# Kernel tuning notes

Measured on AMD Instinct MI355X. Metric: run time of the kernel, lower is better.

Reference implementation:

```python
import jax, jax.numpy as jnp
import numpy as np

N, E, B = 524288, 4194304, 16384
F_IN, FP, TV, GOUT = 14, 1024, 256, 32
EPS = 1e-5
SLOPE = 0.2  # PyG GATConv default negative_slope


def setup_inputs() -> dict:
    key = jax.random.key(0)
    ks = iter(jax.random.split(key, 64))
    def nrm(shape, scale=1.0):
        return jax.random.normal(next(ks), shape, dtype=jnp.float32) * scale
    def uni(shape, lo, hi):
        return jax.random.uniform(next(ks), shape, dtype=jnp.float32, minval=lo, maxval=hi)
    def bn(d):  # [gamma, beta, running_mean, running_var]
        return jnp.stack([uni((d,), 0.5, 1.5), nrm((d,), 0.1), nrm((d,), 0.1), uni((d,), 0.5, 1.5)])
    return {
        'x': nrm((N, F_IN)),
        'edge_index': jax.random.randint(next(ks), (2, E), 0, N, dtype=jnp.int32),
        'batch': jnp.sort(jax.random.randint(next(ks), (N,), 0, B, dtype=jnp.int32)),
        'fingerprint': nrm((B, FP)),
        'transformer_features': nrm((B, TV)),
        'W1': nrm((F_IN, F_IN), 0.3), 'a_src1': nrm((F_IN,), 0.3), 'a_dst1': nrm((F_IN,), 0.3), 'b1': nrm((F_IN,), 0.1),
        'W2': nrm((F_IN, GOUT), 0.3), 'a_src2': nrm((GOUT,), 0.3), 'a_dst2': nrm((GOUT,), 0.3), 'b2': nrm((GOUT,), 0.1),
        'fc1_w': nrm((FP, 400), 0.04), 'fc1_b': nrm((400,), 0.1), 'bn1': bn(400),
        'fc2_w': nrm((400, 200), 0.07), 'fc2_b': nrm((200,), 0.1), 'bn2': bn(200),
        'fc3_w': nrm((TV, 400), 0.08), 'fc3_b': nrm((400,), 0.1), 'bn3': bn(400),
        'fc4_w': nrm((400, 200), 0.07), 'fc4_b': nrm((200,), 0.1), 'bn4': bn(200),
        'fcc1_w': nrm((GOUT + 400, 100), 0.07), 'fcc1_b': nrm((100,), 0.1), 'bnc': bn(100),
        'fcc2_w': nrm((100, 1), 0.1), 'fcc2_b': nrm((1,), 0.1),
    }


def _bn(h, p):  # eval-mode BatchNorm1d with packed params [4, d]
    return (h - p[2]) * jax.lax.rsqrt(p[3] + EPS) * p[0] + p[1]


def _gat(x, W, a_s, a_d, b, src, dst, n):
    # PyG GATConv, heads=1: messages flow src -> dst, softmax over incoming edges per dst
    h = x @ W                                   # [n, C]
    e = jax.nn.leaky_relu((h @ a_s)[src] + (h @ a_d)[dst], SLOPE)  # [E_tot]
    m = jax.lax.stop_gradient(jax.ops.segment_max(e, dst, num_segments=n))
    w = jnp.exp(e - m[dst])
    denom = jax.ops.segment_sum(w, dst, num_segments=n)
    alpha = w / denom[dst]
    out = jax.ops.segment_sum(alpha[:, None] * h[src], dst, num_segments=n)
    return out + b


def reference(x, edge_index, batch, fingerprint, transformer_features,
              W1, a_src1, a_dst1, b1, W2, a_src2, a_dst2, b2,
              fc1_w, fc1_b, bn1, fc2_w, fc2_b, bn2,
              fc3_w, fc3_b, bn3, fc4_w, fc4_b, bn4,
              fcc1_w, fcc1_b, bnc, fcc2_w, fcc2_b):
    n = x.shape[0]
    loop = jnp.arange(n, dtype=edge_index.dtype)  # add_self_loops
    src = jnp.concatenate([edge_index[0], loop])
    dst = jnp.concatenate([edge_index[1], loop])
    g = jax.nn.relu(_gat(x, W1, a_src1, a_dst1, b1, src, dst, n))
    g = jax.nn.relu(_gat(g, W2, a_src2, a_dst2, b2, src, dst, n))
    pool = jax.ops.segment_sum(g, batch, num_segments=B)  # global_add_pool -> [B, GOUT]
    fp = jax.nn.relu(_bn(fingerprint @ fc1_w + fc1_b, bn1))
    fp = jax.nn.relu(_bn(fp @ fc2_w + fc2_b, bn2))
    tv = jax.nn.relu(_bn(transformer_features @ fc3_w + fc3_b, bn3))
    tv = jax.nn.relu(_bn(tv @ fc4_w + fc4_b, bn4))
    comb = jnp.concatenate([pool, fp, tv], axis=1)  # [B, 32+200+200]
    comb = jax.nn.relu(_bn(comb @ fcc1_w + fcc1_b, bnc))
    return comb @ fcc2_w + fcc2_b  # [B, 1]
```

## Files before the change

kernel.cpp:

```cpp
#include <hip/hip_runtime.h>

typedef unsigned short u16;
typedef unsigned int u32;
typedef __attribute__((ext_vector_type(8))) short bf16x8;
typedef __attribute__((ext_vector_type(4))) float f32x4;

#define N_NODES 524288
#define N_EDGES 4194304
#define N_GRAPH 16384
#define P_BLOCKS 1024
#define BKTS 512
#define DPB 1024
#define CAP 8960

__device__ __forceinline__ float bf2f(u16 u){ u32 x=((u32)u)<<16; float f; __builtin_memcpy(&f,&x,4); return f; }
__device__ __forceinline__ float lo2f(u32 u){ u32 x=u<<16; float f; __builtin_memcpy(&f,&x,4); return f; }
__device__ __forceinline__ float hi2f(u32 u){ u32 x=u&0xffff0000u; float f; __builtin_memcpy(&f,&x,4); return f; }
__device__ __forceinline__ u16 f2bf(float f){ u32 x; __builtin_memcpy(&x,&f,4); return (u16)((x + 0x7fffu + ((x>>16)&1u))>>16); }
__device__ __forceinline__ float lrelu(float e){ return e>0.f? e : 0.2f*e; }
__device__ __forceinline__ float gload(const void* p, int i, int is32){
    return is32 ? ((const float*)p)[i] : bf2f(((const u16*)p)[i]);
}
__device__ __forceinline__ u32 fmax_key(float f){ u32 u; __builtin_memcpy(&u,&f,4); return (u>>31)? ~u : (u|0x80000000u); }
__device__ __forceinline__ float key_fmax(u32 k){ u32 u = (k>>31)? (k^0x80000000u) : ~k; float f; __builtin_memcpy(&f,&u,4); return f; }

__device__ __forceinline__ void edge_acc(uint4 q0, uint4 q1, float adv, float M,
        float* acc, float& den){
    float as_; __builtin_memcpy(&as_, &q1.w, 4);
    float w = __expf(lrelu(as_ + adv) - M); den += w;
    u32 u[7] = {q0.x,q0.y,q0.z,q0.w,q1.x,q1.y,q1.z};
    #pragma unroll
    for (int f=0;f<14;f++){ u32 uu=u[f>>1]; acc[f] += w*((f&1)? hi2f(uu):lo2f(uu)); }
}

__device__ __forceinline__ void walk8(const int* __restrict__ ssrc, const u16* __restrict__ hsrc,
        int beg, int end, float adv, float M, float* acc, float& den){
    for (int j = beg; j < end; j += 8){
        int s8[8];
        #pragma unroll
        for (int k=0;k<8;k++){
            int e = j + k;
            s8[k] = __builtin_nontemporal_load(ssrc + ((e < end) ? e : (end-1)));
        }
        uint4 r0[8], r1[8];
        #pragma unroll
        for (int k=0;k<8;k++){
            const uint4* hp = (const uint4*)(hsrc + (size_t)s8[k]*16);
            r0[k] = hp[0]; r1[k] = hp[1];
        }
        int m = end - j;
        #pragma unroll
        for (int k=0;k<8;k++) if (k < m) edge_acc(r0[k], r1[k], adv, M, acc, den);
    }
}

__global__ __launch_bounds__(256) void k_detect(const u32* __restrict__ x, int* __restrict__ flag,
        const void* __restrict__ W2, const void* __restrict__ asw, const void* __restrict__ adw,
        float* __restrict__ prep){
    __shared__ int cnt, s32;
    int t = threadIdx.x;
    if (t==0) cnt = 0;
    __syncthreads();
    int c = 0;
    for (int i = t; i < 1024; i += 256){
        u32 e = (x[i] >> 7) & 0xFF;
        if (e >= 110 && e <= 140) c++;
    }
    atomicAdd(&cnt, c);
    __syncthreads();
    if (t==0){ int f = (cnt < 512) ? 1 : 0; *flag = f; s32 = f; }
    __syncthreads();
    int is32 = s32;
    if (t < 28){
        int j = t % 14, which = t / 14;
        const void* av = which ? adw : asw;
        float s = 0.f;
        #pragma unroll
        for (int k=0;k<32;k++) s += gload(W2, j*32+k, is32) * gload(av, k, is32);
        prep[which*14 + j] = s;
    }
}

__global__ __launch_bounds__(256) void k_cast(const void* __restrict__ in, u16* __restrict__ out,
        int n8, const int* __restrict__ flag){
    int is32 = *flag;
    int idx = blockIdx.x*256 + threadIdx.x;
    if (idx >= n8) return;
    if (is32){
        const float4* ip = (const float4*)in + idx*2;
        float4 a0 = ip[0], a1 = ip[1];
        u32 w0 = (u32)f2bf(a0.x) | ((u32)f2bf(a0.y)<<16);
        u32 w1 = (u32)f2bf(a0.z) | ((u32)f2bf(a0.w)<<16);
        u32 w2 = (u32)f2bf(a1.x) | ((u32)f2bf(a1.y)<<16);
        u32 w3 = (u32)f2bf(a1.z) | ((u32)f2bf(a1.w)<<16);
        ((uint4*)out)[idx] = make_uint4(w0,w1,w2,w3);
    } else {
        ((uint4*)out)[idx] = ((const uint4*)in)[idx];
    }
}

__global__ __launch_bounds__(256) void k_p1(const int* __restrict__ dst, u32* __restrict__ tbl_bm){
    __shared__ u32 lh[BKTS];
    int t = threadIdx.x, blk = blockIdx.x;
    lh[t] = 0; lh[t+256] = 0;
    __syncthreads();
    int base = blk*4096;
    #pragma unroll
    for (int k=0;k<16;k++){
        int d = __builtin_nontemporal_load(dst + base + k*256 + t) & (N_NODES-1);
        atomicAdd(&lh[d>>10], 1);
    }
    __syncthreads();
    tbl_bm[blk*BKTS + t]       = lh[t];
    tbl_bm[blk*BKTS + t + 256] = lh[t+256];
}

__global__ __launch_bounds__(256) void k_ttbl(const u32* __restrict__ bm, u32* __restrict__ km){
    __shared__ u32 tile[32][33];
    int bx = blockIdx.x, by = blockIdx.y;
    int tx = threadIdx.x & 31, ty = threadIdx.x >> 5;
    #pragma unroll
    for (int r=0;r<32;r+=8)
        tile[ty+r][tx] = bm[(bx*32 + ty + r)*BKTS + by*32 + tx];
    __syncthreads();
    #pragma unroll
    for (int r=0;r<32;r+=8)
        km[(by*32 + ty + r)*P_BLOCKS + bx*32 + tx] = tile[tx][ty+r];
}

__global__ __launch_bounds__(256) void k_scan1(int* __restrict__ data, int* __restrict__ bsums){
    __shared__ int sh[256];
    int b = blockIdx.x, t = threadIdx.x;
    int base = b*1024 + t*4;
    int4 v = *(const int4*)(data + base);
    int s = v.x+v.y+v.z+v.w;
    sh[t] = s; __syncthreads();
    for (int off=1; off<256; off<<=1){
        int xv = (t>=off)? sh[t-off] : 0; __syncthreads();
        sh[t] += xv; __syncthreads();
    }
    int excl = sh[t] - s;
    if (t==255) bsums[b] = sh[255];
    int4 o; o.x = excl; o.y = excl+v.x; o.z = o.y+v.y; o.w = o.z+v.z;
    *(int4*)(data + base) = o;
}

__global__ __launch_bounds__(256) void k_scan2(int* __restrict__ bsums){
    __shared__ int sh[256];
    int t = threadIdx.x;
    int v0 = bsums[2*t], v1 = bsums[2*t+1];
    int s = v0+v1; sh[t] = s; __syncthreads();
    for (int off=1; off<256; off<<=1){
        int xv = (t>=off)? sh[t-off] : 0; __syncthreads();
        sh[t] += xv; __syncthreads();
    }
    int excl = sh[t] - s;
    bsums[2*t] = excl; bsums[2*t+1] = excl + v0;
}

__global__ __launch_bounds__(256) void k_scan3(int* __restrict__ scan, const int* __restrict__ bsums, int N_, int E_){
    int i = blockIdx.x*256 + threadIdx.x;
    if (i < N_) scan[i] += bsums[i>>10];
    if (i == 0) scan[N_] = E_;
}

__global__ __launch_bounds__(256) void k_p2(const int* __restrict__ src, const int* __restrict__ dst,
        const u32* __restrict__ km, u32* __restrict__ btab){
    __shared__ u32 lh[BKTS], lofs[BKTS], gofs[BKTS];
    __shared__ u32 stage[4096], tgt[4096];
    __shared__ u32 red[256];
    int t = threadIdx.x, blk = blockIdx.x;
    lh[t] = 0; lh[t+256] = 0;
    __syncthreads();
    u32 pr[16], rk[16]; u16 bk[16];
    int base = blk*4096;
    #pragma unroll
    for (int k=0;k<16;k++){
        int e = base + k*256 + t;
        int d = __builtin_nontemporal_load(dst+e) & (N_NODES-1);
        int s = __builtin_nontemporal_load(src+e) & (N_NODES-1);
        u32 b = (u32)d >> 10;
        bk[k] = (u16)b;
        pr[k] = (u32)(d & 1023) | ((u32)s << 10);
        rk[k] = atomicAdd(&lh[b], 1);
    }
    gofs[t]       = km[(size_t)t*P_BLOCKS + blk];
    gofs[t+256]   = km[(size_t)(t+256)*P_BLOCKS + blk];
    __syncthreads();
    u32 v0 = lh[2*t], v1 = lh[2*t+1];
    u32 s2 = v0+v1; red[t] = s2; __syncthreads();
    for (int off=1; off<256; off<<=1){
        u32 xv = (t>=off)? red[t-off] : 0; __syncthreads();
        red[t] += xv; __syncthreads();
    }
    u32 excl = red[t] - s2;
    lofs[2*t] = excl; lofs[2*t+1] = excl + v0;
    __syncthreads();
    #pragma unroll
    for (int k=0;k<16;k++){
        u32 p = lofs[bk[k]] + rk[k];
        stage[p] = pr[k];
        tgt[p]   = gofs[bk[k]] + rk[k];
    }
    __syncthreads();
    #pragma unroll
    for (int k=0;k<16;k++){
        int j = k*256 + t;
        btab[tgt[j]] = stage[j];
    }
}

__global__ __launch_bounds__(256) void k_p3(const u32* __restrict__ km, const u32* __restrict__ btab,
        int* __restrict__ rowptr, int* __restrict__ ssrc){
    __shared__ u32 fh[DPB], fo[DPB];
    __shared__ u32 red[256];
    __shared__ int sst[CAP];
    int t = threadIdx.x, b = blockIdx.x;
    u32 basep = km[(size_t)b*P_BLOCKS];
    u32 endp  = km[(size_t)(b+1)*P_BLOCKS];
    int cnt = (int)(endp - basep);
    #pragma unroll
    for (int i=t;i<DPB;i+=256) fh[i] = 0;
    __syncthreads();
    for (int j=t; j<cnt; j+=256){
        u32 p = btab[basep + j];
        atomicAdd(&fh[p & 1023], 1);
    }
    __syncthreads();
    u32 v0=fh[4*t], v1=fh[4*t+1], v2=fh[4*t+2], v3=fh[4*t+3];
    u32 s4 = v0+v1+v2+v3; red[t] = s4; __syncthreads();
    for (int off=1; off<256; off<<=1){
        u32 xv = (t>=off)? red[t-off] : 0; __syncthreads();
        red[t] += xv; __syncthreads();
    }
    u32 excl = red[t] - s4;
    fo[4*t]=excl; fo[4*t+1]=excl+v0; fo[4*t+2]=excl+v0+v1; fo[4*t+3]=excl+v0+v1+v2;
    __syncthreads();
    #pragma unroll
    for (int i=t;i<DPB;i+=256) rowptr[b*DPB + i] = (int)(basep + fo[i]);
    if (b == BKTS-1 && t == 0) rowptr[N_NODES] = (int)endp;
    __syncthreads();
    for (int j=t; j<cnt; j+=256){
        u32 p = btab[basep + j];
        u32 pos = atomicAdd(&fo[p & 1023], 1);
        if (pos < (u32)CAP) sst[pos] = (int)(p >> 10);
    }
    __syncthreads();
    for (int j=t; j<cnt; j+=256) ssrc[basep + j] = sst[j];
}

__global__ __launch_bounds__(256) void k_linear1(const void* __restrict__ x,
        const void* __restrict__ W1, const void* __restrict__ asw, const void* __restrict__ adw,
        u16* __restrict__ h1, float* __restrict__ ad1, u32* __restrict__ gkey,
        const int* __restrict__ flag){
    int is32 = *flag;
    __shared__ float Wf[196], av[14], dv[14];
    __shared__ float red[256];
    int t = threadIdx.x;
    if (t < 196) Wf[t] = gload(W1, t, is32);
    else if (t < 210) av[t-196] = gload(asw, t-196, is32);
    else if (t < 224) dv[t-210] = gload(adw, t-210, is32);
    __syncthreads();
    int i = blockIdx.x*256 + t;
    float xv[14];
    if (is32){
        const float* xr = (const float*)x + (size_t)i*14;
        #pragma unroll
        for (int k=0;k<14;k++) xv[k] = xr[k];
    } else {
        const u32* xr = (const u32*)((const u16*)x + (size_t)i*14);
        #pragma unroll
        for (int p=0;p<7;p++){ u32 u = xr[p]; xv[2*p]=lo2f(u); xv[2*p+1]=hi2f(u); }
    }
    float h[14];
    #pragma unroll
    for (int j=0;j<14;j++){ float s=0.f;
        #pragma unroll
        for (int k=0;k<14;k++) s += xv[k]*Wf[k*14+j];
        h[j]=s; }
    float a=0.f, d=0.f;
    #pragma unroll
    for (int j=0;j<14;j++){ a += h[j]*av[j]; d += h[j]*dv[j]; }
    ad1[i]=d;
    u32 ou[8];
    #pragma unroll
    for (int p=0;p<7;p++) ou[p] = (u32)f2bf(h[2*p]) | ((u32)f2bf(h[2*p+1])<<16);
    __builtin_memcpy(&ou[7], &a, 4);
    uint4* hp = (uint4*)(h1 + (size_t)i*16);
    hp[0] = make_uint4(ou[0],ou[1],ou[2],ou[3]);
    hp[1] = make_uint4(ou[4],ou[5],ou[6],ou[7]);
    red[t] = a; __syncthreads();
    for (int o=128;o;o>>=1){ if (t<o) red[t]=fmaxf(red[t],red[t+o]); __syncthreads(); }
    if (t==0) atomicMax(gkey, fmax_key(red[0]));
}

__global__ __launch_bounds__(256) void k_gather1(const int* __restrict__ rowptr, const int* __restrict__ ssrc,
        const u16* __restrict__ h1, const float* __restrict__ ad1, const u32* __restrict__ gkey1,
        const void* __restrict__ b1, const float* __restrict__ prep,
        u16* __restrict__ g1, float* __restrict__ ad2, u32* __restrict__ gkey2,
        const int* __restrict__ flag){
    int is32 = *flag;
    __shared__ float b1s[14], vas[14], vds[14];
    __shared__ float red[256];
    int t = threadIdx.x;
    if (t < 14) b1s[t] = gload(b1, t, is32);
    else if (t < 28) vas[t-14] = prep[t-14];
    else if (t < 42) vds[t-28] = prep[t-28+14];
    __syncthreads();
    int i = blockIdx.x*256 + t;
    float adv = ad1[i];
    float M = lrelu(key_fmax(*gkey1) + adv);
    int beg = rowptr[i], end = rowptr[i+1];
    float acc[14] = {0,0,0,0,0,0,0,0,0,0,0,0,0,0};
    float den = 0.f;
    {
        const uint4* hp = (const uint4*)(h1 + (size_t)i*16);
        edge_acc(hp[0], hp[1], adv, M, acc, den);
    }
    walk8(ssrc, h1, beg, end, adv, M, acc, den);
    float inv = 1.0f/den;
    float v[14];
    #pragma unroll
    for (int f=0;f<14;f++) v[f] = fmaxf(acc[f]*inv + b1s[f], 0.f);
    float a2=0.f, d2=0.f;
    #pragma unroll
    for (int f=0;f<14;f++){ a2 += v[f]*vas[f]; d2 += v[f]*vds[f]; }
    ad2[i] = d2;
    u32 ou[8];
    #pragma unroll
    for (int p=0;p<7;p++) ou[p] = (u32)f2bf(v[2*p]) | ((u32)f2bf(v[2*p+1])<<16);
    __builtin_memcpy(&ou[7], &a2, 4);
    uint4* gp = (uint4*)(g1 + (size_t)i*16);
    gp[0]=make_uint4(ou[0],ou[1],ou[2],ou[3]);
    gp[1]=make_uint4(ou[4],ou[5],ou[6],ou[7]);
    red[t] = a2; __syncthreads();
    for (int o=128;o;o>>=1){ if (t<o) red[t]=fmaxf(red[t],red[t+o]); __syncthreads(); }
    if (t==0) atomicMax(gkey2, fmax_key(red[0]));
}

__global__ __launch_bounds__(256) void k_gather2(const int* __restrict__ rowptr, const int* __restrict__ ssrc,
        const u16* __restrict__ g1, const float* __restrict__ ad2, const u32* __restrict__ gkey2,
        const void* __restrict__ W2, const void* __restrict__ b2, u16* __restrict__ g2,
        const int* __restrict__ flag){
    int is32 = *flag;
    __shared__ float W2s[448], b2s[32];
    int t = threadIdx.x;
    for (int idx=t; idx<448; idx+=256) W2s[idx] = gload(W2, idx, is32);
    if (t < 32) b2s[t] = gload(b2, t, is32);
    __syncthreads();
    int i = blockIdx.x*256 + t;
    float adv = ad2[i];
    float M = lrelu(key_fmax(*gkey2) + adv);
    int beg = rowptr[i], end = rowptr[i+1];
    float acc[14] = {0,0,0,0,0,0,0,0,0,0,0,0,0,0};
    float den = 0.f;
    {
        const uint4* hp = (const uint4*)(g1 + (size_t)i*16);
        edge_acc(hp[0], hp[1], adv, M, acc, den);
    }
    walk8(ssrc, g1, beg, end, adv, M, acc, den);
    float inv = 1.0f/den;
    float an[14];
    #pragma unroll
    for (int f=0;f<14;f++) an[f] = acc[f]*inv;
    uint4* orow = (uint4*)(g2 + (size_t)i*32);
    #pragma unroll
    for (int g=0; g<4; g++){
        u32 ou[4];
        #pragma unroll
        for (int p=0;p<4;p++){
            int j0 = g*8 + 2*p;
            float va_ = b2s[j0], vb_ = b2s[j0+1];
            #pragma unroll
            for (int k=0;k<14;k++){ va_ += an[k]*W2s[k*32+j0]; vb_ += an[k]*W2s[k*32+j0+1]; }
            va_ = fmaxf(va_, 0.f); vb_ = fmaxf(vb_, 0.f);
            ou[p] = (u32)f2bf(va_) | ((u32)f2bf(vb_)<<16);
        }
        orow[g] = make_uint4(ou[0],ou[1],ou[2],ou[3]);
    }
}

__device__ __forceinline__ int lbound(const int* __restrict__ a, int n, int v){
    int lo=0, hi=n;
    while (lo < hi){ int m = (lo+hi)>>1; if (a[m] < v) lo = m+1; else hi = m; }
    return lo;
}

__global__ __launch_bounds__(64) void k_pool(const u16* __restrict__ g2, const int* __restrict__ batch,
        u16* __restrict__ comb, int N_){
    int b = blockIdx.x;
    int t = threadIdx.x, f = t & 31, half = t >> 5;
    int lo = lbound(batch, N_, b);
    int hi = lbound(batch, N_, b+1);
    float acc = 0.f;
    for (int i = lo + half; i < hi; i += 2) acc += bf2f(g2[(size_t)i*32 + f]);
    acc += __shfl_xor(acc, 32);
    if (t < 32) comb[(size_t)b*432 + f] = f2bf(acc);
}

__global__ __launch_bounds__(256) void k_transpose(const void* __restrict__ W, u16* __restrict__ Wt,
        int K, int Kp, int Nc, const int* __restrict__ flag){
    int is32 = *flag;
    int idx = blockIdx.x*256 + threadIdx.x;
    if (idx >= Nc*Kp) return;
    int n = idx / Kp, k = idx - n*Kp;
    Wt[idx] = (k < K) ? f2bf(gload(W, k*Nc + n, is32)) : (u16)0;
}

__global__ __launch_bounds__(256) void k_gemm(const void* __restrict__ A, const u16* __restrict__ Wt,
        const void* __restrict__ bias, const void* __restrict__ bnp, void* __restrict__ out,
        int K, int Kp, int Nc, int ostride, int ooff, int do_relu,
        int out32, const int* __restrict__ flag){
    int is32 = *flag;
    __shared__ u16 As[128][40];
    __shared__ u16 Bs[128][40];
    int t = threadIdx.x;
    int lane = t & 63, wave = t >> 6;
    int bm = blockIdx.x * 128;
    int bn = blockIdx.y * 128;
    int mt = (wave & 1) * 64, nt = (wave >> 1) * 64;
    int quad = lane >> 4, fr = lane & 15;

    f32x4 zero = {0.f, 0.f, 0.f, 0.f};
    f32x4 acc[4][4];
    #pragma unroll
    for (int i=0;i<4;i++)
        #pragma unroll
        for (int j=0;j<4;j++) acc[i][j] = zero;

    int srow0 = t >> 2;
    int scol = (t & 3) * 8;

    for (int k0 = 0; k0 < Kp; k0 += 32){
        #pragma unroll
        for (int h2_=0; h2_<2; h2_++){
            int row = srow0 + h2_*64;
            int gk = k0 + scol;
            uint4 av = make_uint4(0,0,0,0);
            if (gk + 8 <= K) av = *(const uint4*)((const u16*)A + (size_t)(bm+row)*K + gk);
            *(uint4*)(&As[row][scol]) = av;
            uint4 bv = make_uint4(0,0,0,0);
            if (bn + row < Nc) bv = *(const uint4*)(Wt + (size_t)(bn+row)*Kp + gk);
            *(uint4*)(&Bs[row][scol]) = bv;
        }
        __syncthreads();
        bf16x8 af[4], bfr[4];
        #pragma unroll
        for (int i=0;i<4;i++) af[i] = *(const bf16x8*)(&As[mt + i*16 + fr][quad*8]);
        #pragma unroll
        for (int j=0;j<4;j++) bfr[j] = *(const bf16x8*)(&Bs[nt + j*16 + fr][quad*8]);
        #pragma unroll
        for (int i=0;i<4;i++)
            #pragma unroll
            for (int j=0;j<4;j++)
                acc[i][j] = __builtin_amdgcn_mfma_f32_16x16x32_bf16(af[i], bfr[j], acc[i][j], 0, 0, 0);
        __syncthreads();
    }

    #pragma unroll
    for (int j=0;j<4;j++){
        int gn = bn + nt + j*16 + fr;
        if (gn >= Nc) continue;
        float bb = gload(bias, gn, is32);
        float scale = 1.f, shift = bb;
        if (bnp){
            float gm_ = gload(bnp, gn, is32), bt = gload(bnp, Nc+gn, is32);
            float mn = gload(bnp, 2*Nc+gn, is32), vr = gload(bnp, 3*Nc+gn, is32);
            scale = gm_ * rsqrtf(vr + 1e-5f);
            shift = (bb - mn)*scale + bt;
        }
        #pragma unroll
        for (int i=0;i<4;i++){
            #pragma unroll
            for (int r=0;r<4;r++){
                int gm = bm + mt + i*16 + quad*4 + r;
                float v = acc[i][j][r]*scale + shift;
                if (do_relu) v = fmaxf(v, 0.f);
                size_t oidx = (size_t)gm*ostride + ooff + gn;
                if (out32) ((float*)out)[oidx] = v;
                else       ((u16*)out)[oidx] = f2bf(v);
            }
        }
    }
}

__global__ __launch_bounds__(256) void k_fcc2(const float* __restrict__ c1, const void* __restrict__ w,
        const void* __restrict__ b, float* __restrict__ outp, const int* __restrict__ flag){
    int is32 = *flag;
    __shared__ float wf[100];
    int t = threadIdx.x;
    if (t < 100) wf[t] = gload(w, t, is32);
    __syncthreads();
    int i = blockIdx.x*256 + t;
    const float* r = c1 + (size_t)i*100;
    float s = 0.f;
    #pragma unroll 4
    for (int k=0;k<100;k++) s += r[k]*wf[k];
    outp[i] = s + gload(b, 0, is32);
}

extern "C" void kernel_launch(void* const* d_in, const int* in_sizes, int n_in,
                              void* d_out, int out_size, void* d_ws, size_t ws_size,
                              hipStream_t stream){
    const int N = N_NODES, E = N_EDGES;
    const void* x    = d_in[0];
    const int* ei   = (const int*)d_in[1];
    const int* srcA = ei;
    const int* dstA = ei + E;
    const int* batch= (const int*)d_in[2];
    const void* fing = d_in[3];
    const void* tv   = d_in[4];
    const void* W1   = d_in[5];
    const void* as1w = d_in[6];
    const void* ad1w = d_in[7];
    const void* b1   = d_in[8];
    const void* W2   = d_in[9];
    const void* as2w = d_in[10];
    const void* ad2w = d_in[11];
    const void* b2   = d_in[12];
    const void* fc1w = d_in[13]; const void* fc1b = d_in[14]; const void* bn1 = d_in[15];
    const void* fc2w = d_in[16]; const void* fc2b = d_in[17]; const void* bn2 = d_in[18];
    const void* fc3w = d_in[19]; const void* fc3b = d_in[20]; const void* bn3 = d_in[21];
    const void* fc4w = d_in[22]; const void* fc4b = d_in[23]; const void* bn4 = d_in[24];
    const void* fccw = d_in[25]; const void* fccb = d_in[26]; const void* bnc = d_in[27];
    const void* fcc2w= d_in[28]; const void* fcc2b= d_in[29];

    char* ws = (char*)d_ws;
    size_t off = 0;
    auto alloc = [&](size_t bytes)->char*{ char* p = ws + off; off = (off + bytes + 255) & ~(size_t)255; return p; };
    int*  flagp  = (int*)alloc(256);
    u32*  gkey1  = (u32*)flagp + 1;
    u32*  gkey2  = (u32*)flagp + 2;
    float* prep  = (float*)((char*)flagp + 16);
    int*  rowptr = (int*)alloc((size_t)(N+1)*4);
    int*  bsums  = (int*)alloc(513*4);
    u32*  tbl_bm = (u32*)alloc((size_t)BKTS*P_BLOCKS*4);
    u32*  tbl_km = (u32*)alloc(((size_t)BKTS*P_BLOCKS+1)*4);
    int*  ssrc   = (int*)alloc((size_t)E*4);
    u16*  h1     = (u16*)alloc((size_t)N*16*2);
    u16*  g1     = (u16*)alloc((size_t)N*16*2);
    float* ad1_  = (float*)alloc((size_t)N*4);
    float* ad2_  = (float*)alloc((size_t)N*4);
    char* scr32  = alloc((size_t)N*32*2);
    float* c1    = (float*)alloc((size_t)N_GRAPH*100*4);
    u16*  Wt1    = (u16*)alloc((size_t)400*1024*2);
    u16*  Wt2    = (u16*)alloc((size_t)200*416*2);
    u16*  Wt3    = (u16*)alloc((size_t)400*256*2);
    u16*  Wt4    = (u16*)alloc((size_t)200*416*2);
    u16*  Wtc    = (u16*)alloc((size_t)100*448*2);
    u16*  tv_bf  = (u16*)alloc((size_t)N_GRAPH*256*2);
    u32*  btab   = (u32*)scr32;
    u16*  g2     = (u16*)scr32;
    u16*  fp1    = (u16*)scr32;
    u16*  tv1    = (u16*)scr32 + (size_t)N_GRAPH*400;
    u16*  comb   = (u16*)ssrc;
    u16*  fing_bf= h1;

    (void)hipMemsetAsync(flagp, 0, 256, stream);

    k_detect <<<1, 256, 0, stream>>>((const u32*)x, flagp, W2, as2w, ad2w, prep);
    k_cast   <<<(N_GRAPH*256/8+255)/256, 256, 0, stream>>>(tv, tv_bf, N_GRAPH*256/8, flagp);

    k_p1   <<<P_BLOCKS, 256, 0, stream>>>(dstA, tbl_bm);
    k_ttbl <<<dim3(32,16), 256, 0, stream>>>(tbl_bm, tbl_km);
    k_scan1<<<512,  256, 0, stream>>>((int*)tbl_km, bsums);
    k_scan2<<<1,    256, 0, stream>>>(bsums);
    k_scan3<<<(BKTS*P_BLOCKS)/256, 256, 0, stream>>>((int*)tbl_km, bsums, BKTS*P_BLOCKS, E);
    k_p2   <<<P_BLOCKS, 256, 0, stream>>>(srcA, dstA, tbl_km, btab);
    k_p3   <<<BKTS, 256, 0, stream>>>(tbl_km, btab, rowptr, ssrc);

    k_linear1<<<N/256, 256, 0, stream>>>(x, W1, as1w, ad1w, h1, ad1_, gkey1, flagp);
    k_gather1<<<N/256, 256, 0, stream>>>(rowptr, ssrc, h1, ad1_, gkey1, b1, prep, g1, ad2_, gkey2, flagp);
    k_gather2<<<N/256, 256, 0, stream>>>(rowptr, ssrc, g1, ad2_, gkey2, W2, b2, g2, flagp);
    k_cast   <<<(N_GRAPH*1024/8+255)/256, 256, 0, stream>>>(fing, fing_bf, N_GRAPH*1024/8, flagp);
    k_pool   <<<N_GRAPH, 64, 0, stream>>>(g2, batch, comb, N);

    k_transpose<<<(400*1024+255)/256, 256, 0, stream>>>(fc1w, Wt1, 1024, 1024, 400, flagp);
    k_transpose<<<(200*416 +255)/256, 256, 0, stream>>>(fc2w, Wt2,  400,  416, 200, flagp);
    k_transpose<<<(400*256 +255)/256, 256, 0, stream>>>(fc3w, Wt3,  256,  256, 400, flagp);
    k_transpose<<<(200*416 +255)/256, 256, 0, stream>>>(fc4w, Wt4,  400,  416, 200, flagp);
    k_transpose<<<(100*448 +255)/256, 256, 0, stream>>>(fccw, Wtc,  432,  448, 100, flagp);

    k_gemm<<<dim3(128,4), 256, 0, stream>>>(fing_bf, Wt1, fc1b, bn1, fp1, 1024, 1024, 400, 400,   0, 1, 0, flagp);
    k_gemm<<<dim3(128,2), 256, 0, stream>>>(fp1,  Wt2, fc2b, bn2, comb, 400,  416, 200, 432,  32, 1, 0, flagp);
    k_gemm<<<dim3(128,4), 256, 0, stream>>>(tv_bf, Wt3, fc3b, bn3, tv1, 256,  256, 400, 400,   0, 1, 0, flagp);
    k_gemm<<<dim3(128,2), 256, 0, stream>>>(tv1,  Wt4, fc4b, bn4, comb, 400,  416, 200, 432, 232, 1, 0, flagp);
    k_gemm<<<dim3(128,1), 256, 0, stream>>>(comb, Wtc, fccb, bnc, c1,   432,  448, 100, 100,   0, 1, 1, flagp);

    k_fcc2<<<N_GRAPH/256, 256, 0, stream>>>(c1, fcc2w, fcc2b, (float*)d_out, flagp);
}
```

Measured before the change: 727.5 us.

## Co-schedule first MLP GEMMs inside the GAT gather kernel and batch transposes

The fc1 and fc3 GEMMs now run as extra blocks interleaved in the first GAT gather launch (every third block does a GEMM tile). Their A operands are converted from fp32 to bf16 while loading into shared memory, so the separate cast kernels go away. The five weight-transpose launches are merged into one kernel. The aim is to fill the latency-bound gather with compute work and cut launch count. The cost is extra registers and shared memory per gather block, which may lower its occupancy, and fp1/tv1 now need their own buffers.

```diff
diff --git a/kernel.cpp b/kernel.cpp
--- a/kernel.cpp
+++ b/kernel.cpp
@@ -54,6 +54,90 @@
     }
 }
 
+__device__ __forceinline__ void gemm_block(u16 (*As)[40], u16 (*Bs)[40],
+        const void* __restrict__ A, const u16* __restrict__ Wt,
+        const void* __restrict__ bias, const void* __restrict__ bnp, void* __restrict__ out,
+        int K, int Kp, int Nc, int ostride, int ooff, int do_relu,
+        int out32, int araw, int is32, int bm, int bn, int t){
+    int af32 = araw && is32;
+    int lane = t & 63, wave = t >> 6;
+    int mt = (wave & 1) * 64, nt = (wave >> 1) * 64;
+    int quad = lane >> 4, fr = lane & 15;
+
+    f32x4 zero = {0.f, 0.f, 0.f, 0.f};
+    f32x4 acc[4][4];
+    #pragma unroll
+    for (int i=0;i<4;i++)
+        #pragma unroll
+        for (int j=0;j<4;j++) acc[i][j] = zero;
+
+    int srow0 = t >> 2;
+    int scol = (t & 3) * 8;
+
+    for (int k0 = 0; k0 < Kp; k0 += 32){
+        #pragma unroll
+        for (int h2_=0; h2_<2; h2_++){
+            int row = srow0 + h2_*64;
+            int gk = k0 + scol;
+            uint4 av = make_uint4(0,0,0,0);
+            if (gk + 8 <= K){
+                if (af32){
+                    const float* ap = (const float*)A + (size_t)(bm+row)*K + gk;
+                    float4 a0 = *(const float4*)ap, a1 = *(const float4*)(ap+4);
+                    av.x = (u32)f2bf(a0.x) | ((u32)f2bf(a0.y)<<16);
+                    av.y = (u32)f2bf(a0.z) | ((u32)f2bf(a0.w)<<16);
+                    av.z = (u32)f2bf(a1.x) | ((u32)f2bf(a1.y)<<16);
+                    av.w = (u32)f2bf(a1.z) | ((u32)f2bf(a1.w)<<16);
+                } else {
+                    av = *(const uint4*)((const u16*)A + (size_t)(bm+row)*K + gk);
+                }
+            }
+            *(uint4*)(&As[row][scol]) = av;
+            uint4 bv = make_uint4(0,0,0,0);
+            if (bn + row < Nc) bv = *(const uint4*)(Wt + (size_t)(bn+row)*Kp + gk);
+            *(uint4*)(&Bs[row][scol]) = bv;
+        }
+        __syncthreads();
+        bf16x8 af[4], bfr[4];
+        #pragma unroll
+        for (int i=0;i<4;i++) af[i] = *(const bf16x8*)(&As[mt + i*16 + fr][quad*8]);
+        #pragma unroll
+        for (int j=0;j<4;j++) bfr[j] = *(const bf16x8*)(&Bs[nt + j*16 + fr][quad*8]);
+        #pragma unroll
+        for (int i=0;i<4;i++)
+            #pragma unroll
+            for (int j=0;j<4;j++)
+                acc[i][j] = __builtin_amdgcn_mfma_f32_16x16x32_bf16(af[i], bfr[j], acc[i][j], 0, 0, 0);
+        __syncthreads();
+    }
+
+    #pragma unroll
+    for (int j=0;j<4;j++){
+        int gn = bn + nt + j*16 + fr;
+        if (gn >= Nc) continue;
+        float bb = gload(bias, gn, is32);
+        float scale = 1.f, shift = bb;
+        if (bnp){
+            float gm_ = gload(bnp, gn, is32), bt = gload(bnp, Nc+gn, is32);
+            float mn = gload(bnp, 2*Nc+gn, is32), vr = gload(bnp, 3*Nc+gn, is32);
+            scale = gm_ * rsqrtf(vr + 1e-5f);
+            shift = (bb - mn)*scale + bt;
+        }
+        #pragma unroll
+        for (int i=0;i<4;i++){
+            #pragma unroll
+            for (int r=0;r<4;r++){
+                int gm = bm + mt + i*16 + quad*4 + r;
+                float v = acc[i][j][r]*scale + shift;
+                if (do_relu) v = fmaxf(v, 0.f);
+                size_t oidx = (size_t)gm*ostride + ooff + gn;
+                if (out32) ((float*)out)[oidx] = v;
+                else       ((u16*)out)[oidx] = f2bf(v);
+            }
+        }
+    }
+}
+
 __global__ __launch_bounds__(256) void k_detect(const u32* __restrict__ x, int* __restrict__ flag,
         const void* __restrict__ W2, const void* __restrict__ asw, const void* __restrict__ adw,
         float* __restrict__ prep){
@@ -78,24 +162,6 @@
         #pragma unroll
         for (int k=0;k<32;k++) s += gload(W2, j*32+k, is32) * gload(av, k, is32);
         prep[which*14 + j] = s;
-    }
-}
-
-__global__ __launch_bounds__(256) void k_cast(const void* __restrict__ in, u16* __restrict__ out,
-        int n8, const int* __restrict__ flag){
-    int is32 = *flag;
-    int idx = blockIdx.x*256 + threadIdx.x;
-    if (idx >= n8) return;
-    if (is32){
-        const float4* ip = (const float4*)in + idx*2;
-        float4 a0 = ip[0], a1 = ip[1];
-        u32 w0 = (u32)f2bf(a0.x) | ((u32)f2bf(a0.y)<<16);
-        u32 w1 = (u32)f2bf(a0.z) | ((u32)f2bf(a0.w)<<16);
-        u32 w2 = (u32)f2bf(a1.x) | ((u32)f2bf(a1.y)<<16);
-        u32 w3 = (u32)f2bf(a1.z) | ((u32)f2bf(a1.w)<<16);
-        ((uint4*)out)[idx] = make_uint4(w0,w1,w2,w3);
-    } else {
-        ((uint4*)out)[idx] = ((const uint4*)in)[idx];
     }
 }
 
@@ -294,20 +360,39 @@
     if (t==0) atomicMax(gkey, fmax_key(red[0]));
 }
 
-__global__ __launch_bounds__(256) void k_gather1(const int* __restrict__ rowptr, const int* __restrict__ ssrc,
+__global__ __launch_bounds__(256) void k_g1mlp(const int* __restrict__ rowptr, const int* __restrict__ ssrc,
         const u16* __restrict__ h1, const float* __restrict__ ad1, const u32* __restrict__ gkey1,
         const void* __restrict__ b1, const float* __restrict__ prep,
         u16* __restrict__ g1, float* __restrict__ ad2, u32* __restrict__ gkey2,
-        const int* __restrict__ flag){
-    int is32 = *flag;
+        const int* __restrict__ flag,
+        const void* __restrict__ fing, const u16* __restrict__ Wt1,
+        const void* __restrict__ fc1b, const void* __restrict__ bn1, u16* __restrict__ fp1,
+        const void* __restrict__ tv, const u16* __restrict__ Wt3,
+        const void* __restrict__ fc3b, const void* __restrict__ bn3, u16* __restrict__ tv1){
+    __shared__ u16 As[128][40];
+    __shared__ u16 Bs[128][40];
     __shared__ float b1s[14], vas[14], vds[14];
     __shared__ float red[256];
-    int t = threadIdx.x;
+    int is32 = *flag;
+    int bid = blockIdx.x, t = threadIdx.x;
+    if (bid % 3 == 0){
+        int g = bid / 3;
+        if (g < 512){
+            gemm_block(As, Bs, fing, Wt1, fc1b, bn1, fp1, 1024, 1024, 400, 400, 0, 1, 0,
+                       1, is32, (g & 127)*128, (g >> 7)*128, t);
+        } else {
+            g -= 512;
+            gemm_block(As, Bs, tv, Wt3, fc3b, bn3, tv1, 256, 256, 400, 400, 0, 1, 0,
+                       1, is32, (g & 127)*128, (g >> 7)*128, t);
+        }
+        return;
+    }
+    int gb = bid - bid/3 - 1;
     if (t < 14) b1s[t] = gload(b1, t, is32);
     else if (t < 28) vas[t-14] = prep[t-14];
     else if (t < 42) vds[t-28] = prep[t-28+14];
     __syncthreads();
-    int i = blockIdx.x*256 + t;
+    int i = gb*256 + t;
     float adv = ad1[i];
     float M = lrelu(key_fmax(*gkey1) + adv);
     int beg = rowptr[i], end = rowptr[i+1];
@@ -398,90 +483,34 @@
     if (t < 32) comb[(size_t)b*432 + f] = f2bf(acc);
 }
 
-__global__ __launch_bounds__(256) void k_transpose(const void* __restrict__ W, u16* __restrict__ Wt,
-        int K, int Kp, int Nc, const int* __restrict__ flag){
+__global__ __launch_bounds__(256) void k_tall(
+        const void* __restrict__ Wa, const void* __restrict__ Wb, const void* __restrict__ Wc,
+        const void* __restrict__ Wd, const void* __restrict__ We,
+        u16* __restrict__ Ta, u16* __restrict__ Tb, u16* __restrict__ Tc,
+        u16* __restrict__ Td, u16* __restrict__ Te, const int* __restrict__ flag){
     int is32 = *flag;
-    int idx = blockIdx.x*256 + threadIdx.x;
-    if (idx >= Nc*Kp) return;
-    int n = idx / Kp, k = idx - n*Kp;
-    Wt[idx] = (k < K) ? f2bf(gload(W, k*Nc + n, is32)) : (u16)0;
+    int loc = blockIdx.x*256 + threadIdx.x;
+    const int n1=400*1024, n2=200*416, n3=400*256, n4=200*416, n5=100*448;
+    const void* W; u16* T; int K, Kp, Nc;
+    if (loc < n1){ W=Wa; T=Ta; K=1024; Kp=1024; Nc=400; }
+    else if ((loc-=n1) < n2){ W=Wb; T=Tb; K=400; Kp=416; Nc=200; }
+    else if ((loc-=n2) < n3){ W=Wc; T=Tc; K=256; Kp=256; Nc=400; }
+    else if ((loc-=n3) < n4){ W=Wd; T=Td; K=400; Kp=416; Nc=200; }
+    else if ((loc-=n4) < n5){ W=We; T=Te; K=432; Kp=448; Nc=100; }
+    else return;
+    int n = loc / Kp, k = loc - n*Kp;
+    T[loc] = (k < K) ? f2bf(gload(W, k*Nc + n, is32)) : (u16)0;
 }
 
 __global__ __launch_bounds__(256) void k_gemm(const void* __restrict__ A, const u16* __restrict__ Wt,
         const void* __restrict__ bias, const void* __restrict__ bnp, void* __restrict__ out,
         int K, int Kp, int Nc, int ostride, int ooff, int do_relu,
-        int out32, const int* __restrict__ flag){
-    int is32 = *flag;
+        int out32, int araw, const int* __restrict__ flag){
     __shared__ u16 As[128][40];
     __shared__ u16 Bs[128][40];
-    int t = threadIdx.x;
-    int lane = t & 63, wave = t >> 6;
-    int bm = blockIdx.x * 128;
-    int bn = blockIdx.y * 128;
-    int mt = (wave & 1) * 64, nt = (wave >> 1) * 64;
-    int quad = lane >> 4, fr = lane & 15;
-
-    f32x4 zero = {0.f, 0.f, 0.f, 0.f};
-    f32x4 acc[4][4];
-    #pragma unroll
-    for (int i=0;i<4;i++)
-        #pragma unroll
-        for (int j=0;j<4;j++) acc[i][j] = zero;
-
-    int srow0 = t >> 2;
-    int scol = (t & 3) * 8;
-
-    for (int k0 = 0; k0 < Kp; k0 += 32){
-        #pragma unroll
-        for (int h2_=0; h2_<2; h2_++){
-            int row = srow0 + h2_*64;
-            int gk = k0 + scol;
-            uint4 av = make_uint4(0,0,0,0);
-            if (gk + 8 <= K) av = *(const uint4*)((const u16*)A + (size_t)(bm+row)*K + gk);
-            *(uint4*)(&As[row][scol]) = av;
-            uint4 bv = make_uint4(0,0,0,0);
-            if (bn + row < Nc) bv = *(const uint4*)(Wt + (size_t)(bn+row)*Kp + gk);
-            *(uint4*)(&Bs[row][scol]) = bv;
-        }
-        __syncthreads();
-        bf16x8 af[4], bfr[4];
-        #pragma unroll
-        for (int i=0;i<4;i++) af[i] = *(const bf16x8*)(&As[mt + i*16 + fr][quad*8]);
-        #pragma unroll
-        for (int j=0;j<4;j++) bfr[j] = *(const bf16x8*)(&Bs[nt + j*16 + fr][quad*8]);
-        #pragma unroll
-        for (int i=0;i<4;i++)
-            #pragma unroll
-            for (int j=0;j<4;j++)
-                acc[i][j] = __builtin_amdgcn_mfma_f32_16x16x32_bf16(af[i], bfr[j], acc[i][j], 0, 0, 0);
-        __syncthreads();
-    }
-
-    #pragma unroll
-    for (int j=0;j<4;j++){
-        int gn = bn + nt + j*16 + fr;
-        if (gn >= Nc) continue;
-        float bb = gload(bias, gn, is32);
-        float scale = 1.f, shift = bb;
-        if (bnp){
-            float gm_ = gload(bnp, gn, is32), bt = gload(bnp, Nc+gn, is32);
-            float mn = gload(bnp, 2*Nc+gn, is32), vr = gload(bnp, 3*Nc+gn, is32);
-            scale = gm_ * rsqrtf(vr + 1e-5f);
-            shift = (bb - mn)*scale + bt;
-        }
-        #pragma unroll
-        for (int i=0;i<4;i++){
-            #pragma unroll
-            for (int r=0;r<4;r++){
-                int gm = bm + mt + i*16 + quad*4 + r;
-                float v = acc[i][j][r]*scale + shift;
-                if (do_relu) v = fmaxf(v, 0.f);
-                size_t oidx = (size_t)gm*ostride + ooff + gn;
-                if (out32) ((float*)out)[oidx] = v;
-                else       ((u16*)out)[oidx] = f2bf(v);
-            }
-        }
-    }
+    int is32 = *flag;
+    gemm_block(As, Bs, A, Wt, bias, bnp, out, K, Kp, Nc, ostride, ooff, do_relu, out32,
+               araw, is32, blockIdx.x*128, blockIdx.y*128, threadIdx.x);
 }
 
 __global__ __launch_bounds__(256) void k_fcc2(const float* __restrict__ c1, const void* __restrict__ w,
@@ -548,18 +577,17 @@
     u16*  Wt3    = (u16*)alloc((size_t)400*256*2);
     u16*  Wt4    = (u16*)alloc((size_t)200*416*2);
     u16*  Wtc    = (u16*)alloc((size_t)100*448*2);
-    u16*  tv_bf  = (u16*)alloc((size_t)N_GRAPH*256*2);
+    u16*  fp1    = (u16*)alloc((size_t)N_GRAPH*400*2);
+    u16*  tv1    = (u16*)alloc((size_t)N_GRAPH*400*2);
     u32*  btab   = (u32*)scr32;
     u16*  g2     = (u16*)scr32;
-    u16*  fp1    = (u16*)scr32;
-    u16*  tv1    = (u16*)scr32 + (size_t)N_GRAPH*400;
     u16*  comb   = (u16*)ssrc;
-    u16*  fing_bf= h1;
 
     (void)hipMemsetAsync(flagp, 0, 256, stream);
 
     k_detect <<<1, 256, 0, stream>>>((const u32*)x, flagp, W2, as2w, ad2w, prep);
-    k_cast   <<<(N_GRAPH*256/8+255)/256, 256, 0, stream>>>(tv, tv_bf, N_GRAPH*256/8, flagp);
+    k_tall   <<<(400*1024+200*416+400*256+200*416+100*448+255)/256, 256, 0, stream>>>(
+                 fc1w, fc2w, fc3w, fc4w, fccw, Wt1, Wt2, Wt3, Wt4, Wtc, flagp);
 
     k_p1   <<<P_BLOCKS, 256, 0, stream>>>(dstA, tbl_bm);
     k_ttbl <<<dim3(32,16), 256, 0, stream>>>(tbl_bm, tbl_km);
@@ -570,22 +598,15 @@
     k_p3   <<<BKTS, 256, 0, stream>>>(tbl_km, btab, rowptr, ssrc);
 
     k_linear1<<<N/256, 256, 0, stream>>>(x, W1, as1w, ad1w, h1, ad1_, gkey1, flagp);
-    k_gather1<<<N/256, 256, 0, stream>>>(rowptr, ssrc, h1, ad1_, gkey1, b1, prep, g1, ad2_, gkey2, flagp);
+    k_g1mlp <<<3072, 256, 0, stream>>>(rowptr, ssrc, h1, ad1_, gkey1, b1, prep, g1, ad2_, gkey2, flagp,
+                                       fing, Wt1, fc1b, bn1, fp1,
+                                       tv,   Wt3, fc3b, bn3, tv1);
     k_gather2<<<N/256, 256, 0, stream>>>(rowptr, ssrc, g1, ad2_, gkey2, W2, b2, g2, flagp);
-    k_cast   <<<(N_GRAPH*1024/8+255)/256, 256, 0, stream>>>(fing, fing_bf, N_GRAPH*1024/8, flagp);
     k_pool   <<<N_GRAPH, 64, 0, stream>>>(g2, batch, comb, N);
 
-    k_transpose<<<(400*1024+255)/256, 256, 0, stream>>>(fc1w, Wt1, 1024, 1024, 400, flagp);
-    k_transpose<<<(200*416 +255)/256, 256, 0, stream>>>(fc2w, Wt2,  400,  416, 200, flagp);
-    k_transpose<<<(400*256 +255)/256, 256, 0, stream>>>(fc3w, Wt3,  256,  256, 400, flagp);
-    k_transpose<<<(200*416 +255)/256, 256, 0, stream>>>(fc4w, Wt4,  400,  416, 200, flagp);
-    k_transpose<<<(100*448 +255)/256, 256, 0, stream>>>(fccw, Wtc,  432,  448, 100, flagp);
-
-    k_gemm<<<dim3(128,4), 256, 0, stream>>>(fing_bf, Wt1, fc1b, bn1, fp1, 1024, 1024, 400, 400,   0, 1, 0, flagp);
-    k_gemm<<<dim3(128,2), 256, 0, stream>>>(fp1,  Wt2, fc2b, bn2, comb, 400,  416, 200, 432,  32, 1, 0, flagp);
-    k_gemm<<<dim3(128,4), 256, 0, stream>>>(tv_bf, Wt3, fc3b, bn3, tv1, 256,  256, 400, 400,   0, 1, 0, flagp);
-    k_gemm<<<dim3(128,2), 256, 0, stream>>>(tv1,  Wt4, fc4b, bn4, comb, 400,  416, 200, 432, 232, 1, 0, flagp);
-    k_gemm<<<dim3(128,1), 256, 0, stream>>>(comb, Wtc, fccb, bnc, c1,   432,  448, 100, 100,   0, 1, 1, flagp);
+    k_gemm<<<dim3(128,2), 256, 0, stream>>>(fp1, Wt2, fc2b, bn2, comb, 400, 416, 200, 432,  32, 1, 0, 0, flagp);
+    k_gemm<<<dim3(128,2), 256, 0, stream>>>(tv1, Wt4, fc4b, bn4, comb, 400, 416, 200, 432, 232, 1, 0, 0, flagp);
+    k_gemm<<<dim3(128,1), 256, 0, stream>>>(comb, Wtc, fccb, bnc, c1,  432, 448, 100, 100,   0, 1, 1, 0, flagp);
 
     k_fcc2<<<N_GRAPH/256, 256, 0, stream>>>(c1, fcc2w, fcc2b, (float*)d_out, flagp);
 }
```

New measurement: 672.1 us. -7.6%, faster.
